# Kernel optimization log

Hardware: AMD Instinct MI355X
Metric: run time of the kernel (lower is better)

## Reference

```python
import jax, jax.numpy as jnp
import numpy as np

N = 20000      # nodes
E = 320000     # edges
GD = 256       # g_dim
H = 8          # head_n
D = 32         # head_d
XD = 256       # x_dim
PS = 4         # x_ps
HID = 512      # FF hidden (hardcoded in module)
EPS = 1e-5
SCALE = GD ** -0.5  # note: module scales by g_dim**-0.5, not head_d**-0.5


def layernorm(x, w, b):
    mu = jnp.mean(x, axis=-1, keepdims=True)
    var = jnp.var(x, axis=-1, keepdims=True)
    return (x - mu) * jax.lax.rsqrt(var + EPS) * w + b


def setup_inputs() -> dict:
    key = jax.random.key(0)
    ks = jax.random.split(key, 16)
    inp = {
        "x": jax.random.normal(ks[0], (N, XD, PS, PS), jnp.float32),
        "h": jax.random.normal(ks[1], (N, GD), jnp.float32),
        "src": jax.random.randint(ks[2], (E,), 0, N, jnp.int32),
        "dst": jax.random.randint(ks[3], (E,), 0, N, jnp.int32),
        # xproj conv (kernel covers full patch -> equivalent to a linear)
        "conv_w": jax.random.normal(ks[4], (GD, XD, PS, PS), jnp.float32) * 0.02,
        "conv_b": jnp.zeros((GD,), jnp.float32),
        # GraphT outer LayerNorm
        "norm_w": jnp.ones((GD,), jnp.float32),
        "norm_b": jnp.zeros((GD,), jnp.float32),
        # attention norm_in + projections
        "nin_w": jnp.ones((GD,), jnp.float32),
        "nin_b": jnp.zeros((GD,), jnp.float32),
        "w_qkv": jax.random.normal(ks[5], (3 * H * D, GD), jnp.float32) * 0.02,
        "w_out": jax.random.normal(ks[6], (GD, H * D), jnp.float32) * 0.02,
        "b_out": jnp.zeros((GD,), jnp.float32),
        # FeedForward: LayerNorm + Linear(GD,HID) + GELU + Linear(HID,GD)
        "ffn_w": jnp.ones((GD,), jnp.float32),
        "ffn_b": jnp.zeros((GD,), jnp.float32),
        "w1": jax.random.normal(ks[7], (HID, GD), jnp.float32) * 0.02,
        "b1": jnp.zeros((HID,), jnp.float32),
        "w2": jax.random.normal(ks[8], (GD, HID), jnp.float32) * 0.02,
        "b2": jnp.zeros((GD,), jnp.float32),
    }
    return inp


def reference(x, h, src, dst, conv_w, conv_b, norm_w, norm_b, nin_w, nin_b,
              w_qkv, w_out, b_out, ffn_w, ffn_b, w1, b1, w2, b2):
    # xproj: Conv2d with kernel == full spatial extent -> linear over flattened patch
    xp = x.reshape(N, XD * PS * PS) @ conv_w.reshape(GD, XD * PS * PS).T + conv_b  # [N, GD]

    hn = layernorm(h, norm_w, norm_b)  # GraphT.norm

    # --- GraphAttention ---
    s = layernorm(hn, nin_w, nin_b)                    # norm_in
    qkv = s @ w_qkv.T                                  # [N, 3*H*D]
    q, k, v = jnp.split(qkv, 3, axis=-1)
    q = q.reshape(N, H, D)
    k = k.reshape(N, H, D)
    v = v.reshape(N, H, D)

    # per-edge elementwise attention (DGL u_mul_v), scaled
    att = q[src] * k[dst] * SCALE                      # [E, H, D]
    # edge softmax over incoming edges of each destination, per (h, d) slot
    amax = jax.ops.segment_max(att, dst, num_segments=N)   # [N, H, D]
    e = jnp.exp(att - amax[dst])
    z = jax.ops.segment_sum(e, dst, num_segments=N)
    a = e / z[dst]                                     # [E, H, D]
    # weighted aggregation: sum over edges of v_src * att
    rst = jax.ops.segment_sum(v[src] * a, dst, num_segments=N)  # [N, H, D]

    attn_out = rst.reshape(N, H * D) @ w_out.T + b_out  # to_out (dropout=eval noop)

    # --- FeedForward (norm -> linear -> gelu -> linear) ---
    f = layernorm(attn_out, ffn_w, ffn_b)
    f = jax.nn.gelu(f @ w1.T + b1, approximate=False)
    f = f @ w2.T + b2

    out = f + hn + xp
    return out
```

## Files before the change

### kernel.cpp

```cpp
#include <hip/hip_runtime.h>
#include <hip/hip_bf16.h>
#include <math.h>

typedef __hip_bfloat16 bf16;
typedef __attribute__((ext_vector_type(8))) short bf16x8;
typedef __attribute__((ext_vector_type(4))) float f32x4;

#define N_NODES 20000
#define N_EDGES 320000
#define GD 256
#define HID 512
#define QKV3 768
#define XK 4096
#define SCALE 0.0625f
#define EPS 1e-5f

__device__ __forceinline__ float b2f(bf16 x) { return __bfloat162float(x); }
__device__ __forceinline__ bf16 f2b(float x) { return __float2bfloat16(x); }
__device__ __forceinline__ short f2bs(float x) {
    bf16 b = __float2bfloat16(x);
    union { bf16 b; short s; } u; u.b = b; return u.s;
}
__device__ __forceinline__ float ldf(const void* p, size_t i, int isbf) {
    return isbf ? __bfloat162float(((const bf16*)p)[i]) : ((const float*)p)[i];
}

typedef __attribute__((address_space(3))) void lds_void;
typedef __attribute__((address_space(1))) void glb_void;
__device__ __forceinline__ void gload_lds16(const void* g, void* l) {
    __builtin_amdgcn_global_load_lds((const glb_void*)g, (lds_void*)l, 16, 0, 0);
}

__global__ void detect_kernel(const void* __restrict__ normw, int* __restrict__ flag) {
    if (threadIdx.x == 0) {
        unsigned short u = ((const unsigned short*)normw)[0];
        *flag = (u == 0x3F80) ? 1 : 0;
    }
}

struct ConvArgs {
    const void* src[5];
    bf16* dst[5];
    int n[5];
};
__global__ void conv_bf16_all(ConvArgs a, const int* __restrict__ flag) {
    int i = blockIdx.x * 256 + threadIdx.x;
    int fl = *flag;
    #pragma unroll
    for (int s = 0; s < 5; ++s) {
        if (i < a.n[s]) {
            a.dst[s][i] = f2b(ldf(a.src[s], i, fl));
            return;
        }
        i -= a.n[s];
    }
}

__global__ void count_kernel(const int* __restrict__ dst, int* __restrict__ deg) {
    int e = blockIdx.x * 256 + threadIdx.x;
    if (e < N_EDGES) atomicAdd(&deg[dst[e]], 1);
}

__global__ void scan_kernel(const int* __restrict__ deg, int* __restrict__ offsets,
                            int* __restrict__ cursor) {
    const int T = 1024;
    int t = threadIdx.x;
    int chunk = (N_NODES + T - 1) / T;
    int beg = t * chunk;
    int end = beg + chunk; if (end > N_NODES) end = N_NODES;
    int s = 0;
    for (int i = beg; i < end; ++i) s += deg[i];
    __shared__ int ls[T];
    ls[t] = s;
    __syncthreads();
    for (int off = 1; off < T; off <<= 1) {
        int v = (t >= off) ? ls[t - off] : 0;
        __syncthreads();
        ls[t] += v;
        __syncthreads();
    }
    int run = (t == 0) ? 0 : ls[t - 1];
    for (int i = beg; i < end; ++i) {
        offsets[i] = run; cursor[i] = run; run += deg[i];
    }
    if (t == T - 1) offsets[N_NODES] = run;
}

__global__ void fill_kernel(const int* __restrict__ src, const int* __restrict__ dst,
                            int* __restrict__ cursor, int* __restrict__ ssrc) {
    int e = blockIdx.x * 256 + threadIdx.x;
    if (e < N_EDGES) {
        int p = atomicAdd(&cursor[dst[e]], 1);
        ssrc[p] = src[e];
    }
}

__global__ void ln_fused_kernel(const void* __restrict__ h,
                                const void* __restrict__ nw, const void* __restrict__ nb,
                                const void* __restrict__ iw, const void* __restrict__ ib,
                                float* __restrict__ hn, bf16* __restrict__ s,
                                const int* __restrict__ flag) {
    int wave = threadIdx.x >> 6, lane = threadIdx.x & 63;
    int n = blockIdx.x * 4 + wave;
    int fl = *flag;
    size_t base = (size_t)n * GD;
    float x[4]; float sum = 0.f, sq = 0.f;
    #pragma unroll
    for (int i = 0; i < 4; ++i) {
        x[i] = ldf(h, base + lane + 64 * i, fl);
        sum += x[i]; sq += x[i] * x[i];
    }
    #pragma unroll
    for (int off = 32; off; off >>= 1) { sum += __shfl_xor(sum, off); sq += __shfl_xor(sq, off); }
    float mu = sum * (1.0f / GD);
    float rs = rsqrtf(sq * (1.0f / GD) - mu * mu + EPS);
    float y[4]; float s2 = 0.f, q2 = 0.f;
    #pragma unroll
    for (int i = 0; i < 4; ++i) {
        int j = lane + 64 * i;
        y[i] = (x[i] - mu) * rs * ldf(nw, j, fl) + ldf(nb, j, fl);
        hn[base + j] = y[i];
        s2 += y[i]; q2 += y[i] * y[i];
    }
    #pragma unroll
    for (int off = 32; off; off >>= 1) { s2 += __shfl_xor(s2, off); q2 += __shfl_xor(q2, off); }
    float mu2 = s2 * (1.0f / GD);
    float rs2 = rsqrtf(q2 * (1.0f / GD) - mu2 * mu2 + EPS);
    #pragma unroll
    for (int i = 0; i < 4; ++i) {
        int j = lane + 64 * i;
        s[base + j] = f2b((y[i] - mu2) * rs2 * ldf(iw, j, fl) + ldf(ib, j, fl));
    }
}

__global__ void ln_kernel(const bf16* __restrict__ in,
                          const void* __restrict__ w, const void* __restrict__ b,
                          bf16* __restrict__ out, const int* __restrict__ flag) {
    int wave = threadIdx.x >> 6, lane = threadIdx.x & 63;
    int n = blockIdx.x * 4 + wave;
    int fl = *flag;
    size_t base = (size_t)n * GD;
    float x[4]; float sum = 0.f, sq = 0.f;
    #pragma unroll
    for (int i = 0; i < 4; ++i) {
        x[i] = b2f(in[base + lane + 64 * i]);
        sum += x[i]; sq += x[i] * x[i];
    }
    #pragma unroll
    for (int off = 32; off; off >>= 1) { sum += __shfl_xor(sum, off); sq += __shfl_xor(sq, off); }
    float mu = sum * (1.0f / GD);
    float rs = rsqrtf(sq * (1.0f / GD) - mu * mu + EPS);
    #pragma unroll
    for (int i = 0; i < 4; ++i) {
        int j = lane + 64 * i;
        out[base + j] = f2b((x[i] - mu) * rs * ldf(w, j, fl) + ldf(b, j, fl));
    }
}

__global__ void attn_kernel(const bf16* __restrict__ qkv, const int* __restrict__ offsets,
                            const int* __restrict__ ssrc, bf16* __restrict__ rst) {
    int n = blockIdx.x;
    int j = threadIdx.x;
    float kj = b2f(qkv[(size_t)n * QKV3 + GD + j]) * SCALE;
    int beg = offsets[n], end = offsets[n + 1];
    float m = -INFINITY, l = 0.f, acc = 0.f;
    for (int e = beg; e < end; ++e) {
        int sI = ssrc[e];
        const bf16* qrow = qkv + (size_t)sI * QKV3;
        float a = b2f(qrow[j]) * kj;
        float vv = b2f(qrow[2 * GD + j]);
        float mn = fmaxf(m, a);
        float c = __expf(m - mn);
        float p = __expf(a - mn);
        l = l * c + p;
        acc = acc * c + p * vv;
        m = mn;
    }
    rst[(size_t)n * GD + j] = f2b(end > beg ? acc / l : 0.f);
}

__launch_bounds__(256, 3)
__global__ void xproj_kernel(const float* __restrict__ A, const bf16* __restrict__ B,
                             const float* __restrict__ bias, float* __restrict__ C,
                             const int* __restrict__ flag) {
    if (*flag) return;
    constexpr int BM = 128, BK = 32;
    __shared__ __align__(16) float As[2][BM * BK];
    __shared__ __align__(16) bf16  Bs[2][BM][BK + 8];
    const int m0 = blockIdx.x * BM;
    const int n0 = blockIdx.y * BM;
    const int tid = threadIdx.x;
    const int lane = tid & 63;
    const int wave = tid >> 6;
    const int quad = lane >> 4;
    const int l16 = lane & 15;
    const int wm = (wave & 1) * 64;
    const int wn = (wave >> 1) * 64;
    const int kc = XK / gridDim.z;
    const int kbeg = blockIdx.z * kc;
    const int nt = kc / BK;

    f32x4 acc[4][4] = {};
    int4 breg[2];

    auto stageA = [&](int buf, int k0) {
        #pragma unroll
        for (int s = 0; s < 4; ++s) {
            int row = wave * 32 + s * 8 + (lane >> 3);
            int gslot = (lane & 7) ^ (row & 7);
            int gr = m0 + row; if (gr >= N_NODES) gr = N_NODES - 1;
            gload_lds16(A + (size_t)gr * XK + k0 + gslot * 4,
                        &As[buf][(wave * 4 + s) * 256]);
        }
    };
    auto loadB = [&](int k0) {
        #pragma unroll
        for (int u = 0; u < 2; ++u) {
            int c = tid * 2 + u;
            int row = c >> 2, slot = c & 3;
            breg[u] = *(const int4*)((const char*)B + ((size_t)(n0 + row) * XK + k0) * 2 + slot * 16);
        }
    };
    auto writeB = [&](int buf) {
        #pragma unroll
        for (int u = 0; u < 2; ++u) {
            int c = tid * 2 + u;
            int row = c >> 2, slot = c & 3;
            *(int4*)(&Bs[buf][row][slot * 8]) = breg[u];
        }
    };

    loadB(kbeg);
    stageA(0, kbeg);
    writeB(0);
    __syncthreads();

    int buf = 0;
    for (int t = 0; t < nt; ++t) {
        if (t + 1 < nt) {
            loadB(kbeg + (t + 1) * BK);
            stageA(buf ^ 1, kbeg + (t + 1) * BK);
        }
        const f32x4* ap = (const f32x4*)As[buf];
        bf16x8 af[4], bfm[4];
        #pragma unroll
        for (int i = 0; i < 4; ++i) {
            int r = wm + i * 16 + l16;
            f32x4 a0 = ap[r * 8 + ((quad * 2) ^ (r & 7))];
            f32x4 a1 = ap[r * 8 + ((quad * 2 + 1) ^ (r & 7))];
            bf16x8 v;
            v[0] = f2bs(a0[0]); v[1] = f2bs(a0[1]); v[2] = f2bs(a0[2]); v[3] = f2bs(a0[3]);
            v[4] = f2bs(a1[0]); v[5] = f2bs(a1[1]); v[6] = f2bs(a1[2]); v[7] = f2bs(a1[3]);
            af[i] = v;
        }
        #pragma unroll
        for (int j = 0; j < 4; ++j)
            bfm[j] = *(const bf16x8*)(&Bs[buf][wn + j * 16 + l16][quad * 8]);
        #pragma unroll
        for (int i = 0; i < 4; ++i)
            #pragma unroll
            for (int j = 0; j < 4; ++j)
                acc[i][j] = __builtin_amdgcn_mfma_f32_16x16x32_bf16(af[i], bfm[j], acc[i][j], 0, 0, 0);
        if (t + 1 < nt) writeB(buf ^ 1);
        __syncthreads();
        buf ^= 1;
    }

    #pragma unroll
    for (int i = 0; i < 4; ++i) {
        #pragma unroll
        for (int j = 0; j < 4; ++j) {
            int col = n0 + wn + j * 16 + l16;
            float bv = (blockIdx.z == 0) ? bias[col] : 0.0f;
            #pragma unroll
            for (int r = 0; r < 4; ++r) {
                int gr = m0 + wm + i * 16 + quad * 4 + r;
                if (gr >= N_NODES) continue;
                atomicAdd(&C[(size_t)gr * GD + col], acc[i][j][r] + bv);
            }
        }
    }
}

template<int EPI, int DYNA>
__launch_bounds__(256)
__global__ void gemm_bt(const void* __restrict__ A, const bf16* __restrict__ B,
                        const void* __restrict__ bias, void* __restrict__ Cout,
                        const float* __restrict__ add0, const float* __restrict__ add1,
                        int M, int Nn, int K, const int* __restrict__ flag) {
    const int fl = *flag;
    if (DYNA == 2 && fl == 0) return;
    constexpr int BM = 128, BN = 128, BK = 64, LDW = BK + 8;
    __shared__ bf16 As[BM * LDW];
    __shared__ bf16 Bs[BN * LDW];
    const int m0 = blockIdx.x * BM;
    const int n0 = blockIdx.y * BN;
    const int tid = threadIdx.x;
    const int lane = tid & 63;
    const int wave = tid >> 6;
    const int quad = lane >> 4;
    const int l16 = lane & 15;
    const int wm = (wave & 1) * 64;
    const int wn = (wave >> 1) * 64;

    const int kc = K / gridDim.z;
    const int kbeg = blockIdx.z * kc;
    const int kend = kbeg + kc;

    f32x4 acc[4][4] = {};

    for (int k0 = kbeg; k0 < kend; k0 += BK) {
        #pragma unroll
        for (int p = 0; p < 4; ++p) {
            int l = p * 256 + tid;
            int row = l >> 3;
            int ko = (l & 7) * 8;
            int gr = m0 + row; gr = gr < M ? gr : M - 1;
            if (!DYNA || fl) {
                *(int4*)(&As[row * LDW + ko]) =
                    *(const int4*)((const bf16*)A + (size_t)gr * K + k0 + ko);
            } else {
                const float* Af = (const float*)A + (size_t)gr * K + k0 + ko;
                float4 lo = *(const float4*)(Af);
                float4 hi = *(const float4*)(Af + 4);
                bf16x8 v;
                v[0] = f2bs(lo.x); v[1] = f2bs(lo.y); v[2] = f2bs(lo.z); v[3] = f2bs(lo.w);
                v[4] = f2bs(hi.x); v[5] = f2bs(hi.y); v[6] = f2bs(hi.z); v[7] = f2bs(hi.w);
                *(bf16x8*)(&As[row * LDW + ko]) = v;
            }
            *(int4*)(&Bs[row * LDW + ko]) = *(const int4*)(B + (size_t)(n0 + row) * K + k0 + ko);
        }
        __syncthreads();
        #pragma unroll
        for (int kk = 0; kk < BK; kk += 32) {
            bf16x8 af[4], bfm[4];
            #pragma unroll
            for (int i = 0; i < 4; ++i)
                af[i] = *(const bf16x8*)(&As[(wm + i * 16 + l16) * LDW + kk + quad * 8]);
            #pragma unroll
            for (int j = 0; j < 4; ++j)
                bfm[j] = *(const bf16x8*)(&Bs[(wn + j * 16 + l16) * LDW + kk + quad * 8]);
            #pragma unroll
            for (int i = 0; i < 4; ++i)
                #pragma unroll
                for (int j = 0; j < 4; ++j)
                    acc[i][j] = __builtin_amdgcn_mfma_f32_16x16x32_bf16(af[i], bfm[j], acc[i][j], 0, 0, 0);
        }
        __syncthreads();
    }

    #pragma unroll
    for (int i = 0; i < 4; ++i) {
        #pragma unroll
        for (int j = 0; j < 4; ++j) {
            int col = n0 + wn + j * 16 + l16;
            float bv = bias ? ldf(bias, col, fl) : 0.0f;
            if (EPI == 4 && blockIdx.z != 0) bv = 0.0f;
            #pragma unroll
            for (int r = 0; r < 4; ++r) {
                int gr = m0 + wm + i * 16 + quad * 4 + r;
                if (gr >= M) continue;
                float v = acc[i][j][r] + bv;
                size_t idx = (size_t)gr * Nn + col;
                if (EPI == 2) v = 0.5f * v * (1.0f + erff(v * 0.70710678118f));
                if (EPI == 3) v += add0[idx] + add1[idx];
                if (EPI == 0)      ((float*)Cout)[idx] = v;
                else if (EPI == 3) { if (fl) ((bf16*)Cout)[idx] = f2b(v); else ((float*)Cout)[idx] = v; }
                else if (EPI == 4) atomicAdd(&((float*)Cout)[idx], v);
                else               ((bf16*)Cout)[idx] = f2b(v);
            }
        }
    }
}

extern "C" void kernel_launch(void* const* d_in, const int* in_sizes, int n_in,
                              void* d_out, int out_size, void* d_ws, size_t ws_size,
                              hipStream_t stream) {
    const void* x      = d_in[0];
    const void* h      = d_in[1];
    const int*  src    = (const int*)d_in[2];
    const int*  dst    = (const int*)d_in[3];
    const void* conv_w = d_in[4];
    const void* conv_b = d_in[5];
    const void* norm_w = d_in[6];
    const void* norm_b = d_in[7];
    const void* nin_w  = d_in[8];
    const void* nin_b  = d_in[9];
    const void* w_qkv  = d_in[10];
    const void* w_out  = d_in[11];
    const void* b_out  = d_in[12];
    const void* ffn_w  = d_in[13];
    const void* ffn_b  = d_in[14];
    const void* w1     = d_in[15];
    const void* b1     = d_in[16];
    const void* w2     = d_in[17];
    const void* b2     = d_in[18];

    char* w = (char*)d_ws;
    float* xp   = (float*)w; w += (size_t)N_NODES * GD * 4;
    float* hn   = (float*)w; w += (size_t)N_NODES * GD * 4;
    bf16*  s    = (bf16*)w;  w += (size_t)N_NODES * GD * 2;
    bf16*  qkv  = (bf16*)w;  w += (size_t)N_NODES * QKV3 * 2;
    bf16*  rst  = (bf16*)w;  w += (size_t)N_NODES * GD * 2;
    bf16*  attn = (bf16*)w;  w += (size_t)N_NODES * GD * 2;
    bf16*  cw    = (bf16*)w; w += (size_t)4096 * 256 * 2;
    bf16*  wqkvb = (bf16*)w; w += (size_t)768 * 256 * 2;
    bf16*  woutb = (bf16*)w; w += (size_t)256 * 256 * 2;
    bf16*  w1b   = (bf16*)w; w += (size_t)512 * 256 * 2;
    bf16*  w2b   = (bf16*)w; w += (size_t)256 * 512 * 2;
    int* deg     = (int*)w;  w += (size_t)N_NODES * 4;
    int* cursor  = (int*)w;  w += (size_t)N_NODES * 4;
    int* offsets = (int*)w;  w += (size_t)(N_NODES + 4) * 4;
    int* ssrc    = (int*)w;  w += (size_t)N_EDGES * 4;
    int* flag    = (int*)w;  w += 16;
    bf16* fln = s;
    bf16* f1  = qkv;

    detect_kernel<<<1, 64, 0, stream>>>(norm_w, flag);
    ConvArgs ca;
    ca.src[0] = conv_w; ca.dst[0] = cw;    ca.n[0] = 4096 * 256;
    ca.src[1] = w_qkv;  ca.dst[1] = wqkvb; ca.n[1] = 768 * 256;
    ca.src[2] = w_out;  ca.dst[2] = woutb; ca.n[2] = 256 * 256;
    ca.src[3] = w1;     ca.dst[3] = w1b;   ca.n[3] = 512 * 256;
    ca.src[4] = w2;     ca.dst[4] = w2b;   ca.n[4] = 256 * 512;
    int conv_total = ca.n[0] + ca.n[1] + ca.n[2] + ca.n[3] + ca.n[4];
    conv_bf16_all<<<(conv_total + 255) / 256, 256, 0, stream>>>(ca, flag);

    hipMemsetAsync(deg, 0, N_NODES * sizeof(int), stream);
    count_kernel<<<(N_EDGES + 255) / 256, 256, 0, stream>>>(dst, deg);
    scan_kernel<<<1, 1024, 0, stream>>>(deg, offsets, cursor);
    fill_kernel<<<(N_EDGES + 255) / 256, 256, 0, stream>>>(src, dst, cursor, ssrc);

    ln_fused_kernel<<<N_NODES / 4, 256, 0, stream>>>(h, norm_w, norm_b, nin_w, nin_b, hn, s, flag);

    dim3 blk(256);
    hipMemsetAsync(xp, 0, (size_t)N_NODES * GD * 4, stream);
    xproj_kernel<<<dim3(157, 2, 4), blk, 0, stream>>>((const float*)x, cw, (const float*)conv_b, xp, flag);
    gemm_bt<4, 2><<<dim3(157, 2, 4), blk, 0, stream>>>(x, cw, conv_b, xp, nullptr, nullptr, N_NODES, GD, 4096, flag);
    gemm_bt<1, 0><<<dim3(157, 6), blk, 0, stream>>>(s, wqkvb, nullptr, qkv, nullptr, nullptr, N_NODES, QKV3, GD, flag);
    attn_kernel<<<N_NODES, 256, 0, stream>>>(qkv, offsets, ssrc, rst);
    gemm_bt<1, 0><<<dim3(157, 2), blk, 0, stream>>>(rst, woutb, b_out, attn, nullptr, nullptr, N_NODES, GD, GD, flag);
    ln_kernel<<<N_NODES / 4, 256, 0, stream>>>(attn, ffn_w, ffn_b, fln, flag);
    gemm_bt<2, 0><<<dim3(157, 4), blk, 0, stream>>>(fln, w1b, b1, f1, nullptr, nullptr, N_NODES, HID, GD, flag);
    gemm_bt<3, 0><<<dim3(157, 2), blk, 0, stream>>>(f1, w2b, b2, d_out, xp, hn, N_NODES, GD, HID, flag);
}
```

Before: 1.000 ms.

## Rewrite xproj GEMM with pre-tiled weights, full-N blocks and async LDS pipeline

```diff
diff --git a/kernel.cpp b/kernel.cpp
--- a/kernel.cpp
+++ b/kernel.cpp
@@ -43,13 +43,20 @@
     bf16* dst[5];
     int n[5];
 };
-__global__ void conv_bf16_all(ConvArgs a, const int* __restrict__ flag) {
+__global__ void conv_bf16_all(ConvArgs a, const int* __restrict__ flag, bf16* __restrict__ cwt) {
     int i = blockIdx.x * 256 + threadIdx.x;
     int fl = *flag;
     #pragma unroll
     for (int s = 0; s < 5; ++s) {
         if (i < a.n[s]) {
-            a.dst[s][i] = f2b(ldf(a.src[s], i, fl));
+            float v = ldf(a.src[s], i, fl);
+            a.dst[s][i] = f2b(v);
+            if (s == 0) {
+                int r = i >> 12;
+                int k = i & 4095;
+                int T = k >> 5, slot = (k >> 3) & 3, e = k & 7;
+                cwt[((size_t)T << 13) + (slot << 11) + (r << 3) + e] = f2b(v);
+            }
             return;
         }
         i -= a.n[s];
@@ -179,19 +186,17 @@
     rst[(size_t)n * GD + j] = f2b(end > beg ? acc / l : 0.f);
 }
 
-__launch_bounds__(256, 3)
-__global__ void xproj_kernel(const float* __restrict__ A, const bf16* __restrict__ B,
-                             const float* __restrict__ bias, float* __restrict__ C,
-                             const int* __restrict__ flag) {
+__launch_bounds__(512, 4)
+__global__ void xproj_pipe(const float* __restrict__ A, const bf16* __restrict__ Bt,
+                           const float* __restrict__ bias, float* __restrict__ C,
+                           const int* __restrict__ flag) {
     if (*flag) return;
-    constexpr int BM = 128, BK = 32;
-    __shared__ __align__(16) float As[2][BM * BK];
-    __shared__ __align__(16) bf16  Bs[2][BM][BK + 8];
-    const int m0 = blockIdx.x * BM;
-    const int n0 = blockIdx.y * BM;
-    const int tid = threadIdx.x;
-    const int lane = tid & 63;
-    const int wave = tid >> 6;
+    constexpr int BK = 32;
+    __shared__ __align__(16) float As[2][4096];
+    __shared__ __align__(16) bf16  Bs[2][8192];
+    const int m0 = blockIdx.x * 128;
+    const int lane = threadIdx.x & 63;
+    const int wave = threadIdx.x >> 6;
     const int quad = lane >> 4;
     const int l16 = lane & 15;
     const int wm = (wave & 1) * 64;
@@ -201,48 +206,33 @@
     const int nt = kc / BK;
 
     f32x4 acc[4][4] = {};
-    int4 breg[2];
-
-    auto stageA = [&](int buf, int k0) {
-        #pragma unroll
-        for (int s = 0; s < 4; ++s) {
-            int row = wave * 32 + s * 8 + (lane >> 3);
+
+    auto stage = [&](int buf, int t) {
+        int k0 = kbeg + t * BK;
+        #pragma unroll
+        for (int s = 0; s < 2; ++s) {
+            int ki = wave * 2 + s;
+            int row = ki * 8 + (lane >> 3);
+            int gr = m0 + row; if (gr >= N_NODES) gr = N_NODES - 1;
             int gslot = (lane & 7) ^ (row & 7);
-            int gr = m0 + row; if (gr >= N_NODES) gr = N_NODES - 1;
             gload_lds16(A + (size_t)gr * XK + k0 + gslot * 4,
-                        &As[buf][(wave * 4 + s) * 256]);
+                        (char*)(&As[buf][0]) + ki * 1024);
+        }
+        size_t tb = (size_t)(k0 >> 5) * 16384;
+        #pragma unroll
+        for (int s = 0; s < 2; ++s) {
+            int ki = wave * 2 + s;
+            gload_lds16((const char*)Bt + tb + ki * 1024 + lane * 16,
+                        (char*)(&Bs[buf][0]) + ki * 1024);
         }
     };
-    auto loadB = [&](int k0) {
-        #pragma unroll
-        for (int u = 0; u < 2; ++u) {
-            int c = tid * 2 + u;
-            int row = c >> 2, slot = c & 3;
-            breg[u] = *(const int4*)((const char*)B + ((size_t)(n0 + row) * XK + k0) * 2 + slot * 16);
-        }
-    };
-    auto writeB = [&](int buf) {
-        #pragma unroll
-        for (int u = 0; u < 2; ++u) {
-            int c = tid * 2 + u;
-            int row = c >> 2, slot = c & 3;
-            *(int4*)(&Bs[buf][row][slot * 8]) = breg[u];
-        }
-    };
-
-    loadB(kbeg);
-    stageA(0, kbeg);
-    writeB(0);
-    __syncthreads();
-
-    int buf = 0;
-    for (int t = 0; t < nt; ++t) {
-        if (t + 1 < nt) {
-            loadB(kbeg + (t + 1) * BK);
-            stageA(buf ^ 1, kbeg + (t + 1) * BK);
-        }
-        const f32x4* ap = (const f32x4*)As[buf];
-        bf16x8 af[4], bfm[4];
+
+    auto compute = [&](int buf) {
+        bf16x8 bfm[4];
+        #pragma unroll
+        for (int j = 0; j < 4; ++j)
+            bfm[j] = *(const bf16x8*)(&Bs[buf][quad * 2048 + (wn + j * 16 + l16) * 8]);
+        const f32x4* ap = (const f32x4*)(&As[buf][0]);
         #pragma unroll
         for (int i = 0; i < 4; ++i) {
             int r = wm + i * 16 + l16;
@@ -251,26 +241,32 @@
             bf16x8 v;
             v[0] = f2bs(a0[0]); v[1] = f2bs(a0[1]); v[2] = f2bs(a0[2]); v[3] = f2bs(a0[3]);
             v[4] = f2bs(a1[0]); v[5] = f2bs(a1[1]); v[6] = f2bs(a1[2]); v[7] = f2bs(a1[3]);
-            af[i] = v;
-        }
-        #pragma unroll
-        for (int j = 0; j < 4; ++j)
-            bfm[j] = *(const bf16x8*)(&Bs[buf][wn + j * 16 + l16][quad * 8]);
-        #pragma unroll
-        for (int i = 0; i < 4; ++i)
             #pragma unroll
             for (int j = 0; j < 4; ++j)
-                acc[i][j] = __builtin_amdgcn_mfma_f32_16x16x32_bf16(af[i], bfm[j], acc[i][j], 0, 0, 0);
-        if (t + 1 < nt) writeB(buf ^ 1);
-        __syncthreads();
-        buf ^= 1;
-    }
+                acc[i][j] = __builtin_amdgcn_mfma_f32_16x16x32_bf16(v, bfm[j], acc[i][j], 0, 0, 0);
+        }
+    };
+
+    stage(0, 0);
+    stage(1, 1);
+    for (int t = 0; t < nt - 1; ++t) {
+        asm volatile("s_waitcnt vmcnt(4)" ::: "memory");
+        asm volatile("s_barrier" ::: "memory");
+        compute(t & 1);
+        asm volatile("s_waitcnt lgkmcnt(0)" ::: "memory");
+        __builtin_amdgcn_sched_barrier(0);
+        asm volatile("s_barrier" ::: "memory");
+        if (t + 2 < nt) stage(t & 1, t + 2);
+    }
+    asm volatile("s_waitcnt vmcnt(0)" ::: "memory");
+    asm volatile("s_barrier" ::: "memory");
+    compute((nt - 1) & 1);
 
     #pragma unroll
     for (int i = 0; i < 4; ++i) {
         #pragma unroll
         for (int j = 0; j < 4; ++j) {
-            int col = n0 + wn + j * 16 + l16;
+            int col = wn + j * 16 + l16;
             float bv = (blockIdx.z == 0) ? bias[col] : 0.0f;
             #pragma unroll
             for (int r = 0; r < 4; ++r) {
@@ -404,6 +400,7 @@
     bf16*  rst  = (bf16*)w;  w += (size_t)N_NODES * GD * 2;
     bf16*  attn = (bf16*)w;  w += (size_t)N_NODES * GD * 2;
     bf16*  cw    = (bf16*)w; w += (size_t)4096 * 256 * 2;
+    bf16*  cwt   = (bf16*)w; w += (size_t)4096 * 256 * 2;
     bf16*  wqkvb = (bf16*)w; w += (size_t)768 * 256 * 2;
     bf16*  woutb = (bf16*)w; w += (size_t)256 * 256 * 2;
     bf16*  w1b   = (bf16*)w; w += (size_t)512 * 256 * 2;
@@ -424,7 +421,7 @@
     ca.src[3] = w1;     ca.dst[3] = w1b;   ca.n[3] = 512 * 256;
     ca.src[4] = w2;     ca.dst[4] = w2b;   ca.n[4] = 256 * 512;
     int conv_total = ca.n[0] + ca.n[1] + ca.n[2] + ca.n[3] + ca.n[4];
-    conv_bf16_all<<<(conv_total + 255) / 256, 256, 0, stream>>>(ca, flag);
+    conv_bf16_all<<<(conv_total + 255) / 256, 256, 0, stream>>>(ca, flag, cwt);
 
     hipMemsetAsync(deg, 0, N_NODES * sizeof(int), stream);
     count_kernel<<<(N_EDGES + 255) / 256, 256, 0, stream>>>(dst, deg);
@@ -435,7 +432,7 @@
 
     dim3 blk(256);
     hipMemsetAsync(xp, 0, (size_t)N_NODES * GD * 4, stream);
-    xproj_kernel<<<dim3(157, 2, 4), blk, 0, stream>>>((const float*)x, cw, (const float*)conv_b, xp, flag);
+    xproj_pipe<<<dim3(157, 1, 4), dim3(512), 0, stream>>>((const float*)x, cwt, (const float*)conv_b, xp, flag);
     gemm_bt<4, 2><<<dim3(157, 2, 4), blk, 0, stream>>>(x, cw, conv_b, xp, nullptr, nullptr, N_NODES, GD, 4096, flag);
     gemm_bt<1, 0><<<dim3(157, 6), blk, 0, stream>>>(s, wqkvb, nullptr, qkv, nullptr, nullptr, N_NODES, QKV3, GD, flag);
     attn_kernel<<<N_NODES, 256, 0, stream>>>(qkv, offsets, ssrc, rst);
```

New measurement: 929.7 us. 7.0% less time.
